# Performance work log

Measured on AMD Instinct MI355X. Metric: run time of the kernel, lower is better.

## Reference

```python
import jax, jax.numpy as jnp
import numpy as np

S, B, E, H = 2048, 2, 1024, 16
D = E // H  # head_dim = 64


def setup_inputs() -> dict:
    key = jax.random.key(0)
    ks = jax.random.split(key, 11)
    std = 1.0 / np.sqrt(E)
    return {
        "query": jax.random.normal(ks[0], (S, B, E), jnp.float32),
        "key": jax.random.normal(ks[1], (S, B, E), jnp.float32),
        "value": jax.random.normal(ks[2], (S, B, E), jnp.float32),
        "q_w": jax.random.uniform(ks[3], (E, E), jnp.float32, -std, std),
        "q_b": jax.random.uniform(ks[4], (E,), jnp.float32, -std, std),
        "k_w": jax.random.uniform(ks[5], (E, E), jnp.float32, -std, std),
        "k_b": jax.random.uniform(ks[6], (E,), jnp.float32, -std, std),
        "v_w": jax.random.uniform(ks[7], (E, E), jnp.float32, -std, std),
        "v_b": jax.random.uniform(ks[8], (E,), jnp.float32, -std, std),
        "out_w": jax.random.uniform(ks[9], (E, E), jnp.float32, -std, std),
        "out_b": jax.random.uniform(ks[10], (E,), jnp.float32, -std, std),
    }


def reference(query, key, value, q_w, q_b, k_w, k_b, v_w, v_b, out_w, out_b):
    tgt_len, bsz, embed_dim = query.shape
    src_len = key.shape[0]
    head_dim = embed_dim // H
    scaling = head_dim ** -0.5

    # nn.Linear: x @ W.T + b
    q = (jnp.einsum('sbe,fe->sbf', query, q_w) + q_b) * scaling
    k = jnp.einsum('sbe,fe->sbf', key, k_w) + k_b
    v = jnp.einsum('sbe,fe->sbf', value, v_w) + v_b

    # [S, B, E] -> [B*H, S, D]
    def split_heads(x, n):
        return x.reshape(n, bsz * H, head_dim).transpose(1, 0, 2)

    q = split_heads(q, tgt_len)
    k = split_heads(k, src_len)
    v = split_heads(v, src_len)

    scores = jnp.einsum('bqd,bkd->bqk', q, k)        # [B*H, S, S]
    attn = jax.nn.softmax(scores, axis=-1)            # dropout p=0 -> identity
    out = jnp.einsum('bqk,bkd->bqd', attn, v)         # [B*H, S, D]
    out = out.transpose(1, 0, 2).reshape(tgt_len, bsz, embed_dim)
    Z = jnp.einsum('sbe,fe->sbf', out, out_w) + out_b
    attn_avg = attn.reshape(bsz, H, tgt_len, src_len).sum(axis=1) / H
    return Z, attn_avg
```

## Files before the change

kernel.cpp:

```cpp
#include <hip/hip_runtime.h>
#include <cstdint>
#include <cstddef>

#define S_LEN 2048
#define BATCH 2
#define EMB   1024
#define NHEAD 16
#define HDIM  64

typedef short short8 __attribute__((ext_vector_type(8)));
typedef float f32x4  __attribute__((ext_vector_type(4)));

__device__ __forceinline__ unsigned short f2b(float f) {
    unsigned int u = __float_as_uint(f);
    u = (u + 0x7FFFu + ((u >> 16) & 1u)) >> 16;
    return (unsigned short)u;
}
__device__ __forceinline__ unsigned int pk2(float a, float b) {
    return (unsigned int)f2b(a) | ((unsigned int)f2b(b) << 16);
}
__device__ __forceinline__ float b2f_lo(unsigned int u) { return __uint_as_float(u << 16); }
__device__ __forceinline__ float b2f_hi(unsigned int u) { return __uint_as_float(u & 0xFFFF0000u); }

template<int ABF16>
__device__ __forceinline__ void gemm_body(
    ushort (*As)[64 * 40], ushort (*Bs)[128 * 40],
    const void* __restrict__ A_, const float* __restrict__ W,
    const float* __restrict__ bias, void* __restrict__ out_,
    float scale, int mode)
{
    constexpr int K = EMB;
    constexpr int NT = K / 32;
    constexpr int LDP = 40;

    const int t    = threadIdx.x;
    const int lane = t & 63;
    const int wave = t >> 6;
    const int quad = lane >> 4;
    const int l15  = lane & 15;
    const int wm   = wave >> 2;
    const int wn   = wave & 3;
    const int m0   = blockIdx.x * 64;
    const int n0   = blockIdx.y * 128;

    const int rowA = t >> 3, ka = (t & 7) * 4;
    const int rowW = t >> 2, kw = (t & 3) * 8;

    const float*  Af  = (const float*)A_;
    const ushort* Ab  = (const ushort*)A_;
    const size_t aOff = (size_t)(m0 + rowA) * K + ka;
    const float*  Wp  = W + (size_t)(n0 + rowW) * K + kw;

    f32x4 acc[2][2];
#pragma unroll
    for (int mi = 0; mi < 2; ++mi)
#pragma unroll
        for (int ni = 0; ni < 2; ++ni) acc[mi][ni] = (f32x4){0.f, 0.f, 0.f, 0.f};

    uint2 ua;
    uint4 uw;
    if (ABF16) ua = *(const uint2*)(Ab + aOff);
    else {
        float4 f = *(const float4*)(Af + aOff);
        ua = make_uint2(pk2(f.x, f.y), pk2(f.z, f.w));
    }
    {
        float4 g0 = *(const float4*)(Wp);
        float4 g1 = *(const float4*)(Wp + 4);
        uw = make_uint4(pk2(g0.x,g0.y), pk2(g0.z,g0.w), pk2(g1.x,g1.y), pk2(g1.z,g1.w));
    }
    *(uint2*)&As[0][rowA * LDP + ka] = ua;
    *(uint4*)&Bs[0][rowW * LDP + kw] = uw;
    __syncthreads();

    for (int kt = 0; kt < NT; ++kt) {
        const int cur = kt & 1;
        if (kt + 1 < NT) {
            const int k0 = (kt + 1) * 32;
            if (ABF16) ua = *(const uint2*)(Ab + aOff + k0);
            else {
                float4 f = *(const float4*)(Af + aOff + k0);
                ua = make_uint2(pk2(f.x, f.y), pk2(f.z, f.w));
            }
            float4 g0 = *(const float4*)(Wp + k0);
            float4 g1 = *(const float4*)(Wp + k0 + 4);
            uw = make_uint4(pk2(g0.x,g0.y), pk2(g0.z,g0.w), pk2(g1.x,g1.y), pk2(g1.z,g1.w));
        }
        short8 af[2], bf[2];
#pragma unroll
        for (int mi = 0; mi < 2; ++mi)
            af[mi] = *(const short8*)&As[cur][(wm * 32 + mi * 16 + l15) * LDP + quad * 8];
#pragma unroll
        for (int ni = 0; ni < 2; ++ni)
            bf[ni] = *(const short8*)&Bs[cur][(wn * 32 + ni * 16 + l15) * LDP + quad * 8];
#pragma unroll
        for (int mi = 0; mi < 2; ++mi)
#pragma unroll
            for (int ni = 0; ni < 2; ++ni)
                acc[mi][ni] = __builtin_amdgcn_mfma_f32_16x16x32_bf16(
                    af[mi], bf[ni], acc[mi][ni], 0, 0, 0);
        if (kt + 1 < NT) {
            const int nxt = (kt + 1) & 1;
            *(uint2*)&As[nxt][rowA * LDP + ka] = ua;
            *(uint4*)&Bs[nxt][rowW * LDP + kw] = uw;
            __syncthreads();
        }
    }

#pragma unroll
    for (int mi = 0; mi < 2; ++mi)
#pragma unroll
        for (int ni = 0; ni < 2; ++ni) {
            const int col = n0 + wn * 32 + ni * 16 + l15;
            const float bc = bias[col];
#pragma unroll
            for (int r = 0; r < 4; ++r) {
                const int rg = m0 + wm * 32 + mi * 16 + quad * 4 + r;
                const float v = (acc[mi][ni][r] + bc) * scale;
                if (mode == 0) {
                    ((float*)out_)[(size_t)rg * EMB + col] = v;
                } else {
                    const int s  = rg >> 1;
                    const int bb = rg & 1;
                    const int h  = col >> 6;
                    const int d  = col & 63;
                    if (mode == 1)
                        ((ushort*)out_)[(((size_t)(bb * NHEAD + h)) * S_LEN + s) * HDIM + d] = f2b(v);
                    else
                        ((ushort*)out_)[(((size_t)(bb * NHEAD + h)) * HDIM + d) * S_LEN + s] = f2b(v);
                }
            }
        }
}

__global__ __launch_bounds__(512, 2)
void gemm_qkv(const float* __restrict__ qi, const float* __restrict__ ki,
              const float* __restrict__ vi,
              const float* __restrict__ qW, const float* __restrict__ kW,
              const float* __restrict__ vW,
              const float* __restrict__ qB, const float* __restrict__ kB,
              const float* __restrict__ vB,
              ushort* __restrict__ qO, ushort* __restrict__ kO,
              ushort* __restrict__ vO)
{
    __shared__ ushort As[2][64 * 40];
    __shared__ ushort Bs[2][128 * 40];
    const int z = blockIdx.z;
    const float* A    = (z == 0) ? qi : (z == 1) ? ki : vi;
    const float* W    = (z == 0) ? qW : (z == 1) ? kW : vW;
    const float* bias = (z == 0) ? qB : (z == 1) ? kB : vB;
    ushort* out       = (z == 0) ? qO : (z == 1) ? kO : vO;
    const float scale = (z == 0) ? 0.125f : 1.0f;
    const int   mode  = (z == 2) ? 2 : 1;
    gemm_body<0>(As, Bs, A, W, bias, out, scale, mode);
}

__global__ __launch_bounds__(512, 2)
void gemm_z(const ushort* __restrict__ A, const float* __restrict__ W,
            const float* __restrict__ bias, float* __restrict__ out)
{
    __shared__ ushort As[2][64 * 40];
    __shared__ ushort Bs[2][128 * 40];
    gemm_body<1>(As, Bs, A, W, bias, out, 1.0f, 0);
}

#define PLD 2056
__global__ __launch_bounds__(512, 2)
void attn_bf16(const ushort* __restrict__ qw, const ushort* __restrict__ kw,
               const ushort* __restrict__ vt, ushort* __restrict__ ao,
               ushort* __restrict__ pavg_ws)
{
    __shared__ ushort pLds[16 * PLD];
    __shared__ float  redS[8 * 16];
    __shared__ float  red2[4 * 16 * 16];

    const int t     = threadIdx.x;
    const int lane  = t & 63;
    const int wave  = t >> 6;
    const int quad  = lane >> 4;
    const int l15   = lane & 15;
    const int rbase = quad * 4;

    const int bid     = blockIdx.x;
    const int logical = (bid & 7) * 64 + (bid >> 3);
    const int qt      = logical & 127;
    const int rest    = logical >> 7;
    const int b       = rest & 1;
    const int g       = rest >> 1;
    const int sq0     = qt * 16;

    const int ntile = wave & 3;
    const int khalf = wave >> 2;
    const int colAvg = (wave * 16 + l15) * 16;

    float pavg[4][16];
#pragma unroll
    for (int r = 0; r < 4; ++r)
#pragma unroll
        for (int j = 0; j < 16; ++j) pavg[r][j] = 0.f;

    for (int hh = 0; hh < 8; ++hh) {
        const int h  = g * 8 + hh;
        const int bh = b * NHEAD + h;
        const ushort* qbase = qw + ((size_t)bh * S_LEN + sq0) * HDIM;
        const ushort* kbse  = kw + (size_t)bh * S_LEN * HDIM;

        const short8 qf0 = *(const short8*)(qbase + l15 * HDIM + quad * 8);
        const short8 qf1 = *(const short8*)(qbase + l15 * HDIM + 32 + quad * 8);

        float s4[4] = {0.f, 0.f, 0.f, 0.f};
#pragma unroll
        for (int ti = 0; ti < 16; ++ti) {
            const int c0 = wave * 256 + ti * 16;
            const ushort* kr = kbse + (size_t)(c0 + l15) * HDIM;
            const short8 k0 = *(const short8*)(kr + quad * 8);
            const short8 k1 = *(const short8*)(kr + 32 + quad * 8);
            f32x4 a = (f32x4){0.f, 0.f, 0.f, 0.f};
            a = __builtin_amdgcn_mfma_f32_16x16x32_bf16(qf0, k0, a, 0, 0, 0);
            a = __builtin_amdgcn_mfma_f32_16x16x32_bf16(qf1, k1, a, 0, 0, 0);
#pragma unroll
            for (int r = 0; r < 4; ++r) {
                const float e = exp2f(fmaf(a[r], 1.44269504f, -11.54156035f));
                s4[r] += e;
                pLds[(rbase + r) * PLD + c0 + l15] = f2b(e);
            }
        }
#pragma unroll
        for (int off = 1; off < 16; off <<= 1)
#pragma unroll
            for (int r = 0; r < 4; ++r) s4[r] += __shfl_xor(s4[r], off, 16);
        if (l15 == 0)
#pragma unroll
            for (int r = 0; r < 4; ++r) redS[wave * 16 + rbase + r] = s4[r];
        __syncthreads();

        float rinv[4];
#pragma unroll
        for (int r = 0; r < 4; ++r) {
            float s = redS[rbase + r];
#pragma unroll
            for (int w = 1; w < 8; ++w) s += redS[w * 16 + rbase + r];
            rinv[r] = 1.0f / s;
        }

#pragma unroll
        for (int r = 0; r < 4; ++r) {
            const float ri = rinv[r];
#pragma unroll
            for (int c = 0; c < 2; ++c) {
                const uint4 u = *(const uint4*)&pLds[(rbase + r) * PLD + colAvg + c * 8];
                pavg[r][c * 8 + 0] = fmaf(b2f_lo(u.x), ri, pavg[r][c * 8 + 0]);
                pavg[r][c * 8 + 1] = fmaf(b2f_hi(u.x), ri, pavg[r][c * 8 + 1]);
                pavg[r][c * 8 + 2] = fmaf(b2f_lo(u.y), ri, pavg[r][c * 8 + 2]);
                pavg[r][c * 8 + 3] = fmaf(b2f_hi(u.y), ri, pavg[r][c * 8 + 3]);
                pavg[r][c * 8 + 4] = fmaf(b2f_lo(u.z), ri, pavg[r][c * 8 + 4]);
                pavg[r][c * 8 + 5] = fmaf(b2f_hi(u.z), ri, pavg[r][c * 8 + 5]);
                pavg[r][c * 8 + 6] = fmaf(b2f_lo(u.w), ri, pavg[r][c * 8 + 6]);
                pavg[r][c * 8 + 7] = fmaf(b2f_hi(u.w), ri, pavg[r][c * 8 + 7]);
            }
        }

        const ushort* vrow = vt + ((size_t)bh * HDIM + ntile * 16 + l15) * S_LEN + khalf * 1024;
        const ushort* prow = &pLds[l15 * PLD + khalf * 1024];
        f32x4 o0 = (f32x4){0.f, 0.f, 0.f, 0.f}, o1 = o0;
#pragma unroll
        for (int st = 0; st < 32; st += 2) {
            const short8 pa0 = *(const short8*)(prow + st * 32 + quad * 8);
            const short8 vb0 = *(const short8*)(vrow + st * 32 + quad * 8);
            o0 = __builtin_amdgcn_mfma_f32_16x16x32_bf16(pa0, vb0, o0, 0, 0, 0);
            const short8 pa1 = *(const short8*)(prow + (st + 1) * 32 + quad * 8);
            const short8 vb1 = *(const short8*)(vrow + (st + 1) * 32 + quad * 8);
            o1 = __builtin_amdgcn_mfma_f32_16x16x32_bf16(pa1, vb1, o1, 0, 0, 0);
        }
        const f32x4 o = o0 + o1;
        if (khalf == 1) {
#pragma unroll
            for (int r = 0; r < 4; ++r)
                red2[ntile * 256 + (rbase + r) * 16 + l15] = o[r];
        }
        __syncthreads();
        if (khalf == 0) {
#pragma unroll
            for (int r = 0; r < 4; ++r) {
                const float val = (o[r] + red2[ntile * 256 + (rbase + r) * 16 + l15]) * rinv[r];
                const int s = sq0 + rbase + r;
                const int d = ntile * 16 + l15;
                ao[((size_t)s * BATCH + b) * EMB + h * HDIM + d] = f2b(val);
            }
        }
    }

    const float inv16 = 0.0625f;
#pragma unroll
    for (int r = 0; r < 4; ++r) {
        const int s = sq0 + rbase + r;
        ushort* dst = pavg_ws + (((size_t)(g * BATCH + b)) * S_LEN + s) * S_LEN + colAvg;
#pragma unroll
        for (int c = 0; c < 2; ++c) {
            uint4 u;
            u.x = pk2(pavg[r][c * 8 + 0] * inv16, pavg[r][c * 8 + 1] * inv16);
            u.y = pk2(pavg[r][c * 8 + 2] * inv16, pavg[r][c * 8 + 3] * inv16);
            u.z = pk2(pavg[r][c * 8 + 4] * inv16, pavg[r][c * 8 + 5] * inv16);
            u.w = pk2(pavg[r][c * 8 + 6] * inv16, pavg[r][c * 8 + 7] * inv16);
            *(uint4*)(dst + c * 8) = u;
        }
    }
}

__global__ __launch_bounds__(256)
void avg_reduce(const ushort* __restrict__ p, float* __restrict__ out)
{
    const size_t N = (size_t)BATCH * S_LEN * S_LEN;
    const size_t i = ((size_t)blockIdx.x * 256 + threadIdx.x) * 8;
    const uint4 a = *(const uint4*)(p + i);
    const uint4 c = *(const uint4*)(p + i + N);
    float4 o0 = make_float4(b2f_lo(a.x) + b2f_lo(c.x), b2f_hi(a.x) + b2f_hi(c.x),
                            b2f_lo(a.y) + b2f_lo(c.y), b2f_hi(a.y) + b2f_hi(c.y));
    float4 o1 = make_float4(b2f_lo(a.z) + b2f_lo(c.z), b2f_hi(a.z) + b2f_hi(c.z),
                            b2f_lo(a.w) + b2f_lo(c.w), b2f_hi(a.w) + b2f_hi(c.w));
    *(float4*)(out + i)     = o0;
    *(float4*)(out + i + 4) = o1;
}

extern "C" void kernel_launch(void* const* d_in, const int* in_sizes, int n_in,
                              void* d_out, int out_size, void* d_ws, size_t ws_size,
                              hipStream_t stream)
{
    const float* query = (const float*)d_in[0];
    const float* key   = (const float*)d_in[1];
    const float* value = (const float*)d_in[2];
    const float* q_w   = (const float*)d_in[3];
    const float* q_b   = (const float*)d_in[4];
    const float* k_w   = (const float*)d_in[5];
    const float* k_b   = (const float*)d_in[6];
    const float* v_w   = (const float*)d_in[7];
    const float* v_b   = (const float*)d_in[8];
    const float* out_w = (const float*)d_in[9];
    const float* out_b = (const float*)d_in[10];

    float* Z        = (float*)d_out;
    float* attn_avg = Z + (size_t)S_LEN * BATCH * EMB;

    const size_t QKV = (size_t)S_LEN * BATCH * EMB;
    ushort* q_ws  = (ushort*)d_ws;
    ushort* k_ws  = q_ws + QKV;
    ushort* vt_ws = k_ws + QKV;
    ushort* ao_ws = vt_ws + QKV;
    ushort* pavg_ws = ao_ws + QKV;

    const dim3 blkG(512);
    const dim3 gq(64, 8, 3);
    gemm_qkv<<<gq, blkG, 0, stream>>>(query, key, value, q_w, k_w, v_w,
                                      q_b, k_b, v_b, q_ws, k_ws, vt_ws);

    attn_bf16<<<dim3(512), blkG, 0, stream>>>(q_ws, k_ws, vt_ws, ao_ws, pavg_ws);

    avg_reduce<<<4096, 256, 0, stream>>>(pavg_ws, attn_avg);

    const dim3 gz(64, 8);
    gemm_z<<<gz, blkG, 0, stream>>>(ao_ws, out_w, out_b, Z);
}
```

Before: 485.3 us.

## Pre-cast GEMM operands to bf16 and stage tiles via direct global-to-LDS loads

Adds separate cast kernels that convert the fp32 inputs and weights to bf16 before the projection GEMMs. The GEMM core now stages tiles with global_load_lds straight into XOR-swizzled LDS and uses a 128x128 tile in place of 64x128. This takes the per-tile register conversion and LDS store work out of the GEMM loop and raises data reuse per block. The cost is two extra kernel launches and an extra pass over the inputs and weights in memory. The weight casts are repeated on every call, so there is no caching.

```diff
diff --git a/kernel.cpp b/kernel.cpp
--- a/kernel.cpp
+++ b/kernel.cpp
@@ -22,16 +22,51 @@
 __device__ __forceinline__ float b2f_lo(unsigned int u) { return __uint_as_float(u << 16); }
 __device__ __forceinline__ float b2f_hi(unsigned int u) { return __uint_as_float(u & 0xFFFF0000u); }
 
-template<int ABF16>
-__device__ __forceinline__ void gemm_body(
-    ushort (*As)[64 * 40], ushort (*Bs)[128 * 40],
-    const void* __restrict__ A_, const float* __restrict__ W,
+__device__ __forceinline__ void gload_lds16(const ushort* g, ushort* l) {
+    __builtin_amdgcn_global_load_lds(
+        (const __attribute__((address_space(1))) void*)g,
+        (__attribute__((address_space(3))) void*)l, 16, 0, 0);
+}
+
+__global__ __launch_bounds__(256)
+void cast3(const float* __restrict__ s0, const float* __restrict__ s1,
+           const float* __restrict__ s2, ushort* __restrict__ d0,
+           ushort* __restrict__ d1, ushort* __restrict__ d2)
+{
+    const float* s = (blockIdx.y == 0) ? s0 : (blockIdx.y == 1) ? s1 : s2;
+    ushort*      d = (blockIdx.y == 0) ? d0 : (blockIdx.y == 1) ? d1 : d2;
+    const size_t i = ((size_t)blockIdx.x * 256 + threadIdx.x) * 8;
+    const float4 a = *(const float4*)(s + i);
+    const float4 b = *(const float4*)(s + i + 4);
+    *(uint4*)(d + i) = make_uint4(pk2(a.x, a.y), pk2(a.z, a.w),
+                                  pk2(b.x, b.y), pk2(b.z, b.w));
+}
+
+__global__ __launch_bounds__(256)
+void cast4(const float* __restrict__ s0, const float* __restrict__ s1,
+           const float* __restrict__ s2, const float* __restrict__ s3,
+           ushort* __restrict__ d0, ushort* __restrict__ d1,
+           ushort* __restrict__ d2, ushort* __restrict__ d3)
+{
+    const float* s = (blockIdx.y == 0) ? s0 : (blockIdx.y == 1) ? s1
+                   : (blockIdx.y == 2) ? s2 : s3;
+    ushort*      d = (blockIdx.y == 0) ? d0 : (blockIdx.y == 1) ? d1
+                   : (blockIdx.y == 2) ? d2 : d3;
+    const size_t i = ((size_t)blockIdx.x * 256 + threadIdx.x) * 8;
+    const float4 a = *(const float4*)(s + i);
+    const float4 b = *(const float4*)(s + i + 4);
+    *(uint4*)(d + i) = make_uint4(pk2(a.x, a.y), pk2(a.z, a.w),
+                                  pk2(b.x, b.y), pk2(b.z, b.w));
+}
+
+__device__ __forceinline__ void gemm_core(
+    ushort (*As)[128 * 32], ushort (*Bs)[128 * 32],
+    const ushort* __restrict__ A, const ushort* __restrict__ W,
     const float* __restrict__ bias, void* __restrict__ out_,
     float scale, int mode)
 {
-    constexpr int K = EMB;
+    constexpr int K  = EMB;
     constexpr int NT = K / 32;
-    constexpr int LDP = 40;
 
     const int t    = threadIdx.x;
     const int lane = t & 63;
@@ -40,82 +75,61 @@
     const int l15  = lane & 15;
     const int wm   = wave >> 2;
     const int wn   = wave & 3;
-    const int m0   = blockIdx.x * 64;
+    const int m0   = blockIdx.x * 128;
     const int n0   = blockIdx.y * 128;
 
-    const int rowA = t >> 3, ka = (t & 7) * 4;
-    const int rowW = t >> 2, kw = (t & 3) * 8;
-
-    const float*  Af  = (const float*)A_;
-    const ushort* Ab  = (const ushort*)A_;
-    const size_t aOff = (size_t)(m0 + rowA) * K + ka;
-    const float*  Wp  = W + (size_t)(n0 + rowW) * K + kw;
-
-    f32x4 acc[2][2];
-#pragma unroll
-    for (int mi = 0; mi < 2; ++mi)
+    const int srow = t >> 2;
+    const int sseg = ((t & 3) ^ ((srow >> 1) & 3)) << 3;
+    const ushort* gA = A + (size_t)(m0 + srow) * K + sseg;
+    const ushort* gW = W + (size_t)(n0 + srow) * K + sseg;
+
+    f32x4 acc[4][2];
+#pragma unroll
+    for (int mi = 0; mi < 4; ++mi)
 #pragma unroll
         for (int ni = 0; ni < 2; ++ni) acc[mi][ni] = (f32x4){0.f, 0.f, 0.f, 0.f};
 
-    uint2 ua;
-    uint4 uw;
-    if (ABF16) ua = *(const uint2*)(Ab + aOff);
-    else {
-        float4 f = *(const float4*)(Af + aOff);
-        ua = make_uint2(pk2(f.x, f.y), pk2(f.z, f.w));
-    }
-    {
-        float4 g0 = *(const float4*)(Wp);
-        float4 g1 = *(const float4*)(Wp + 4);
-        uw = make_uint4(pk2(g0.x,g0.y), pk2(g0.z,g0.w), pk2(g1.x,g1.y), pk2(g1.z,g1.w));
-    }
-    *(uint2*)&As[0][rowA * LDP + ka] = ua;
-    *(uint4*)&Bs[0][rowW * LDP + kw] = uw;
+#define STAGE(buf, kt) do {                         \
+        gload_lds16(gA + (kt) * 32, &As[buf][t * 8]); \
+        gload_lds16(gW + (kt) * 32, &Bs[buf][t * 8]); \
+    } while (0)
+
+    STAGE(0, 0);
     __syncthreads();
 
     for (int kt = 0; kt < NT; ++kt) {
         const int cur = kt & 1;
-        if (kt + 1 < NT) {
-            const int k0 = (kt + 1) * 32;
-            if (ABF16) ua = *(const uint2*)(Ab + aOff + k0);
-            else {
-                float4 f = *(const float4*)(Af + aOff + k0);
-                ua = make_uint2(pk2(f.x, f.y), pk2(f.z, f.w));
-            }
-            float4 g0 = *(const float4*)(Wp + k0);
-            float4 g1 = *(const float4*)(Wp + k0 + 4);
-            uw = make_uint4(pk2(g0.x,g0.y), pk2(g0.z,g0.w), pk2(g1.x,g1.y), pk2(g1.z,g1.w));
-        }
-        short8 af[2], bf[2];
-#pragma unroll
-        for (int mi = 0; mi < 2; ++mi)
-            af[mi] = *(const short8*)&As[cur][(wm * 32 + mi * 16 + l15) * LDP + quad * 8];
-#pragma unroll
-        for (int ni = 0; ni < 2; ++ni)
-            bf[ni] = *(const short8*)&Bs[cur][(wn * 32 + ni * 16 + l15) * LDP + quad * 8];
-#pragma unroll
-        for (int mi = 0; mi < 2; ++mi)
+        if (kt + 1 < NT) STAGE(cur ^ 1, kt + 1);
+        short8 af[4], bf[2];
+#pragma unroll
+        for (int mi = 0; mi < 4; ++mi) {
+            const int ra = wm * 64 + mi * 16 + l15;
+            af[mi] = *(const short8*)&As[cur][ra * 32 + ((quad ^ ((ra >> 1) & 3)) << 3)];
+        }
+#pragma unroll
+        for (int ni = 0; ni < 2; ++ni) {
+            const int rb = wn * 32 + ni * 16 + l15;
+            bf[ni] = *(const short8*)&Bs[cur][rb * 32 + ((quad ^ ((rb >> 1) & 3)) << 3)];
+        }
+#pragma unroll
+        for (int mi = 0; mi < 4; ++mi)
 #pragma unroll
             for (int ni = 0; ni < 2; ++ni)
                 acc[mi][ni] = __builtin_amdgcn_mfma_f32_16x16x32_bf16(
                     af[mi], bf[ni], acc[mi][ni], 0, 0, 0);
-        if (kt + 1 < NT) {
-            const int nxt = (kt + 1) & 1;
-            *(uint2*)&As[nxt][rowA * LDP + ka] = ua;
-            *(uint4*)&Bs[nxt][rowW * LDP + kw] = uw;
-            __syncthreads();
-        }
+        __syncthreads();
     }
-
-#pragma unroll
-    for (int mi = 0; mi < 2; ++mi)
+#undef STAGE
+
+#pragma unroll
+    for (int mi = 0; mi < 4; ++mi)
 #pragma unroll
         for (int ni = 0; ni < 2; ++ni) {
             const int col = n0 + wn * 32 + ni * 16 + l15;
             const float bc = bias[col];
 #pragma unroll
             for (int r = 0; r < 4; ++r) {
-                const int rg = m0 + wm * 32 + mi * 16 + quad * 4 + r;
+                const int rg = m0 + wm * 64 + mi * 16 + quad * 4 + r;
                 const float v = (acc[mi][ni][r] + bc) * scale;
                 if (mode == 0) {
                     ((float*)out_)[(size_t)rg * EMB + col] = v;
@@ -134,34 +148,34 @@
 }
 
 __global__ __launch_bounds__(512, 2)
-void gemm_qkv(const float* __restrict__ qi, const float* __restrict__ ki,
-              const float* __restrict__ vi,
-              const float* __restrict__ qW, const float* __restrict__ kW,
-              const float* __restrict__ vW,
+void gemm_qkv(const ushort* __restrict__ qi, const ushort* __restrict__ ki,
+              const ushort* __restrict__ vi,
+              const ushort* __restrict__ qW, const ushort* __restrict__ kW,
+              const ushort* __restrict__ vW,
               const float* __restrict__ qB, const float* __restrict__ kB,
               const float* __restrict__ vB,
               ushort* __restrict__ qO, ushort* __restrict__ kO,
               ushort* __restrict__ vO)
 {
-    __shared__ ushort As[2][64 * 40];
-    __shared__ ushort Bs[2][128 * 40];
+    __shared__ ushort As[2][128 * 32];
+    __shared__ ushort Bs[2][128 * 32];
     const int z = blockIdx.z;
-    const float* A    = (z == 0) ? qi : (z == 1) ? ki : vi;
-    const float* W    = (z == 0) ? qW : (z == 1) ? kW : vW;
-    const float* bias = (z == 0) ? qB : (z == 1) ? kB : vB;
-    ushort* out       = (z == 0) ? qO : (z == 1) ? kO : vO;
-    const float scale = (z == 0) ? 0.125f : 1.0f;
-    const int   mode  = (z == 2) ? 2 : 1;
-    gemm_body<0>(As, Bs, A, W, bias, out, scale, mode);
+    const ushort* A    = (z == 0) ? qi : (z == 1) ? ki : vi;
+    const ushort* W    = (z == 0) ? qW : (z == 1) ? kW : vW;
+    const float* bias  = (z == 0) ? qB : (z == 1) ? kB : vB;
+    ushort* out        = (z == 0) ? qO : (z == 1) ? kO : vO;
+    const float scale  = (z == 0) ? 0.125f : 1.0f;
+    const int   mode   = (z == 2) ? 2 : 1;
+    gemm_core(As, Bs, A, W, bias, out, scale, mode);
 }
 
 __global__ __launch_bounds__(512, 2)
-void gemm_z(const ushort* __restrict__ A, const float* __restrict__ W,
+void gemm_z(const ushort* __restrict__ A, const ushort* __restrict__ W,
             const float* __restrict__ bias, float* __restrict__ out)
 {
-    __shared__ ushort As[2][64 * 40];
-    __shared__ ushort Bs[2][128 * 40];
-    gemm_body<1>(As, Bs, A, W, bias, out, 1.0f, 0);
+    __shared__ ushort As[2][128 * 32];
+    __shared__ ushort Bs[2][128 * 32];
+    gemm_core(As, Bs, A, W, bias, out, 1.0f, 0);
 }
 
 #define PLD 2056
@@ -342,21 +356,31 @@
     float* attn_avg = Z + (size_t)S_LEN * BATCH * EMB;
 
     const size_t QKV = (size_t)S_LEN * BATCH * EMB;
-    ushort* q_ws  = (ushort*)d_ws;
-    ushort* k_ws  = q_ws + QKV;
-    ushort* vt_ws = k_ws + QKV;
-    ushort* ao_ws = vt_ws + QKV;
+    ushort* q_ws    = (ushort*)d_ws;
+    ushort* k_ws    = q_ws + QKV;
+    ushort* vt_ws   = k_ws + QKV;
+    ushort* ao_ws   = vt_ws + QKV;
     ushort* pavg_ws = ao_ws + QKV;
+    ushort* qbf     = pavg_ws + 2 * (size_t)BATCH * S_LEN * S_LEN;
+    ushort* kbf     = qbf + QKV;
+    ushort* vbf     = kbf + QKV;
+    ushort* wqb     = vbf + QKV;
+    ushort* wkb     = wqb + (size_t)EMB * EMB;
+    ushort* wvb     = wkb + (size_t)EMB * EMB;
+    ushort* wob     = wvb + (size_t)EMB * EMB;
+
+    cast3<<<dim3(2048, 3), 256, 0, stream>>>(query, key, value, qbf, kbf, vbf);
+    cast4<<<dim3(512, 4), 256, 0, stream>>>(q_w, k_w, v_w, out_w, wqb, wkb, wvb, wob);
 
     const dim3 blkG(512);
-    const dim3 gq(64, 8, 3);
-    gemm_qkv<<<gq, blkG, 0, stream>>>(query, key, value, q_w, k_w, v_w,
+    const dim3 gq(32, 8, 3);
+    gemm_qkv<<<gq, blkG, 0, stream>>>(qbf, kbf, vbf, wqb, wkb, wvb,
                                       q_b, k_b, v_b, q_ws, k_ws, vt_ws);
 
     attn_bf16<<<dim3(512), blkG, 0, stream>>>(q_ws, k_ws, vt_ws, ao_ws, pavg_ws);
 
     avg_reduce<<<4096, 256, 0, stream>>>(pavg_ws, attn_avg);
 
-    const dim3 gz(64, 8);
-    gemm_z<<<gz, blkG, 0, stream>>>(ao_ws, out_w, out_b, Z);
-}
+    const dim3 gz(32, 8);
+    gemm_z<<<gz, blkG, 0, stream>>>(ao_ws, wob, out_b, Z);
+}
```

Measured after the change: 456.5 us. 5.9% less time.
